# Kernel tuning notes

Hardware: AMD Instinct MI355X
Metric: run time of the kernel (lower is better)

Reference implementation:

```python
import jax, jax.numpy as jnp
import numpy as np

N, D_IN, H, OUT, L = 6144, 512, 512, 256, 3
EPS = 1e-5


def setup_inputs() -> dict:
    key = jax.random.key(0)
    ks = jax.random.split(key, 32)
    inp = {}
    inp["X"] = jax.random.normal(ks[0], (N, D_IN), dtype=jnp.float32)
    inp["adj"] = jax.random.randint(ks[1], (N, N), 0, 2).astype(jnp.float32)
    inp["adj_glo"] = jax.random.randint(ks[2], (N, N), 0, 2).astype(jnp.float32)
    s = 1.0 / np.sqrt(H)
    # projection + its BN
    inp["Wp"] = jax.random.normal(ks[3], (H, D_IN), dtype=jnp.float32) / np.sqrt(D_IN)
    inp["bp"] = jnp.zeros((H,), jnp.float32)
    inp["gp"] = jnp.ones((H,), jnp.float32)
    inp["betap"] = jnp.zeros((H,), jnp.float32)
    # per-layer params; layers 0,1 output H, layer 2 outputs OUT
    outs = [H, H, OUT]
    for i in range(L):
        o = outs[i]
        k = jax.random.split(ks[4 + i], 6)
        inp[f"Wq{i}"] = jax.random.normal(k[0], (H, H), jnp.float32) * s
        inp[f"Wk{i}"] = jax.random.normal(k[1], (H, H), jnp.float32) * s
        inp[f"Wv{i}"] = jax.random.normal(k[2], (H, H), jnp.float32) * s
        inp[f"Wo{i}"] = jax.random.normal(k[3], (o, H), jnp.float32) * s
        inp[f"bo{i}"] = jnp.zeros((o,), jnp.float32)
        inp[f"g{i}"] = jnp.ones((o,), jnp.float32)
        inp[f"beta{i}"] = jnp.zeros((o,), jnp.float32)
    return inp


def _normalize_adj(a):
    # symmetric GCN normalization D^{-1/2} A D^{-1/2}
    d = a.sum(axis=1)
    dis = jnp.where(d > 0, jax.lax.rsqrt(jnp.maximum(d, 1e-12)), 0.0)
    return a * dis[:, None] * dis[None, :]


def _bn(x, g, b):
    # BatchNorm1d, training mode: batch stats, biased variance
    m = x.mean(axis=0)
    v = x.var(axis=0)
    return g * (x - m) * jax.lax.rsqrt(v + EPS) + b


def _attn(h, adj, Wq, Wk, Wv, Wo, bo):
    Q = h @ Wq.T
    K = h @ Wk.T
    V = h @ Wv.T
    scores = (Q @ K.T) / np.sqrt(H)            # [N, N]
    scores = jnp.where(adj == 0, -jnp.inf, scores)
    attn = jax.nn.softmax(scores, axis=-1)
    return (attn @ V) @ Wo.T + bo


def reference(X, adj, adj_glo, Wp, bp, gp, betap,
              Wq0, Wk0, Wv0, Wo0, bo0, g0, beta0,
              Wq1, Wk1, Wv1, Wo1, bo1, g1, beta1,
              Wq2, Wk2, Wv2, Wo2, bo2, g2, beta2):
    # embedding: normalized global adjacency aggregation + projection + BN
    h = _normalize_adj(adj_glo) @ X
    h = h @ Wp.T + bp
    h = _bn(h, gp, betap)
    embed_features = h
    layers = [
        (Wq0, Wk0, Wv0, Wo0, bo0, g0, beta0),
        (Wq1, Wk1, Wv1, Wo1, bo1, g1, beta1),
        (Wq2, Wk2, Wv2, Wo2, bo2, g2, beta2),
    ]
    for i, (Wq, Wk, Wv, Wo, bo, g, b) in enumerate(layers):
        h_s = h
        h = _attn(h, adj, Wq, Wk, Wv, Wo, bo)
        h = jax.nn.relu(_bn(h, g, b))
        if i != L - 1:
            h = h + h_s
    return h, embed_features
```

## Files before the change

### kernel.cpp

```cpp
#include <hip/hip_runtime.h>
#include <cstdint>

#define NROW 6144
#define HDIM 512
#define DOUT 256
#define NEG_INF (-__builtin_inff())

typedef _Float16 half8 __attribute__((ext_vector_type(8)));
typedef _Float16 half4v __attribute__((ext_vector_type(4)));
typedef float f32x4 __attribute__((ext_vector_type(4)));

#define BARRIER() asm volatile("s_barrier" ::: "memory")
#define LGKM0()   asm volatile("s_waitcnt lgkmcnt(0)" ::: "memory")
#define VMCNT4()  asm volatile("s_waitcnt vmcnt(4)" ::: "memory")
#define VMCNT0()  asm volatile("s_waitcnt vmcnt(0)" ::: "memory")

__device__ __forceinline__ void gld_lds16(void* lds, const void* g) {
  __builtin_amdgcn_global_load_lds(
      (const __attribute__((address_space(1))) void*)g,
      (__attribute__((address_space(3))) void*)lds, 16, 0, 0);
}

__global__ __launch_bounds__(512, 2)
void gemm256(const _Float16* __restrict__ A, int lda,
             const _Float16* __restrict__ B, int ldb,
             _Float16* __restrict__ C, int ldc, int Kc, long MN)
{
  __shared__ _Float16 As[2][256][64];
  __shared__ _Float16 Bs[2][256][64];
  const int tid = threadIdx.x;
  const int wave = tid >> 6, lane = tid & 63;
  const int wr = wave >> 2, wc = wave & 3;

  const int gx = gridDim.x, gy = gridDim.y;
  const int nwg = gx * gy * gridDim.z;
  int lin = (blockIdx.z * gy + blockIdx.y) * gx + blockIdx.x;
  int swz = (nwg % 8 == 0) ? ((lin % 8) * (nwg >> 3) + (lin >> 3)) : lin;
  const int bx = swz % gx, by = (swz / gx) % gy, bz = swz / (gx * gy);
  const int row0 = bx * 256, col0 = by * 256;
  const _Float16* Ab = A + (size_t)row0 * lda + (size_t)bz * Kc;
  const _Float16* Bb = B + (size_t)col0 * ldb + (size_t)bz * Kc;
  const int nt = Kc >> 6;

  const int srow = lane >> 3;
  const int sgr  = (lane & 7) ^ srow;

  auto stageA = [&](int buf, int h, int t) {
    const _Float16* src = Ab + (size_t)(h * 128 + wave * 8 + srow) * lda + t * 64 + sgr * 8;
    gld_lds16(&As[buf][h * 128 + wave * 8][0], src);
    gld_lds16(&As[buf][h * 128 + 64 + wave * 8][0], src + (size_t)64 * lda);
  };
  auto stageB = [&](int buf, int h, int t) {
    const _Float16* src = Bb + (size_t)(h * 128 + wave * 8 + srow) * ldb + t * 64 + sgr * 8;
    gld_lds16(&Bs[buf][h * 128 + wave * 8][0], src);
    gld_lds16(&Bs[buf][h * 128 + 64 + wave * 8][0], src + (size_t)64 * ldb);
  };

  const int fr = lane & 15, sq = lane >> 4, fx = fr & 7;
  half8 af[4][2], bLo[2][2], bHi[2][2];
  f32x4 acc[8][4];
  const f32x4 vzero = {0.f, 0.f, 0.f, 0.f};
  #pragma unroll
  for (int f = 0; f < 8; ++f)
    #pragma unroll
    for (int j = 0; j < 4; ++j)
      acc[f][j] = vzero;

  auto dsA = [&](int buf, int mh) {
    #pragma unroll
    for (int i = 0; i < 4; ++i)
      #pragma unroll
      for (int ks = 0; ks < 2; ++ks)
        af[i][ks] = *(const half8*)&As[buf][wr * 128 + mh * 64 + i * 16 + fr]
                                          [((ks * 4 + sq) ^ fx) * 8];
  };
  auto dsBlo = [&](int buf) {
    #pragma unroll
    for (int jj = 0; jj < 2; ++jj)
      #pragma unroll
      for (int ks = 0; ks < 2; ++ks)
        bLo[jj][ks] = *(const half8*)&Bs[buf][wc * 64 + jj * 16 + fr]
                                            [((ks * 4 + sq) ^ fx) * 8];
  };
  auto dsBhi = [&](int buf) {
    #pragma unroll
    for (int jj = 0; jj < 2; ++jj)
      #pragma unroll
      for (int ks = 0; ks < 2; ++ks)
        bHi[jj][ks] = *(const half8*)&Bs[buf][wc * 64 + 32 + jj * 16 + fr]
                                            [((ks * 4 + sq) ^ fx) * 8];
  };
  auto mQlo = [&](int fb) {
    __builtin_amdgcn_s_setprio(1);
    #pragma unroll
    for (int i = 0; i < 4; ++i)
      #pragma unroll
      for (int jj = 0; jj < 2; ++jj)
        #pragma unroll
        for (int ks = 0; ks < 2; ++ks)
          acc[fb + i][jj] = __builtin_amdgcn_mfma_f32_16x16x32_f16(
              af[i][ks], bLo[jj][ks], acc[fb + i][jj], 0, 0, 0);
    __builtin_amdgcn_s_setprio(0);
  };
  auto mQhi = [&](int fb) {
    __builtin_amdgcn_s_setprio(1);
    #pragma unroll
    for (int i = 0; i < 4; ++i)
      #pragma unroll
      for (int jj = 0; jj < 2; ++jj)
        #pragma unroll
        for (int ks = 0; ks < 2; ++ks)
          acc[fb + i][2 + jj] = __builtin_amdgcn_mfma_f32_16x16x32_f16(
              af[i][ks], bHi[jj][ks], acc[fb + i][2 + jj], 0, 0, 0);
    __builtin_amdgcn_s_setprio(0);
  };

  stageA(0, 0, 0); stageA(0, 1, 0); stageB(0, 0, 0); stageB(0, 1, 0);
  stageB(1, 0, 1); stageB(1, 1, 1);
  VMCNT4();
  BARRIER();

  for (int T = 0; T < nt; T += 2) {
    const bool pipe = (T + 2 < nt);
    dsA(0, 0); dsBlo(0);
    stageA(1, 0, T + 1);
    BARRIER(); LGKM0(); mQlo(0); BARRIER();
    dsBhi(0);
    stageA(1, 1, T + 1);
    BARRIER(); LGKM0(); mQhi(0); BARRIER();
    dsA(0, 1);
    if (pipe) stageB(0, 0, T + 2);
    BARRIER(); LGKM0(); mQhi(4); BARRIER();
    if (pipe) { stageB(0, 1, T + 2); VMCNT4(); } else { VMCNT0(); }
    BARRIER(); mQlo(4); BARRIER();
    dsA(1, 0); dsBlo(1);
    if (pipe) stageA(0, 0, T + 2);
    BARRIER(); LGKM0(); mQlo(0); BARRIER();
    dsBhi(1);
    if (pipe) stageA(0, 1, T + 2);
    BARRIER(); LGKM0(); mQhi(0); BARRIER();
    dsA(1, 1);
    if (pipe) stageB(1, 0, T + 3);
    BARRIER(); LGKM0(); mQhi(4); BARRIER();
    if (pipe) { stageB(1, 1, T + 3); VMCNT4(); } else { VMCNT0(); }
    BARRIER(); mQlo(4); BARRIER();
  }

  _Float16* dst = C + (size_t)bz * MN;
  #pragma unroll
  for (int f = 0; f < 8; ++f)
    #pragma unroll
    for (int j = 0; j < 4; ++j)
      #pragma unroll
      for (int r = 0; r < 4; ++r) {
        int row = row0 + wr * 128 + f * 16 + sq * 4 + r;
        int col = col0 + wc * 64 + j * 16 + fr;
        dst[(size_t)row * ldc + col] = (_Float16)acc[f][j][r];
      }
}

__global__ __launch_bounds__(256)
void gemm_f16(const _Float16* __restrict__ A, int lda,
              const _Float16* __restrict__ B, int ldb,
              float* __restrict__ Cf, _Float16* __restrict__ Ch, int ldc,
              int Kc, _Float16* __restrict__ Pk, long MN)
{
  __shared__ _Float16 As[128][32];
  __shared__ _Float16 Bs[128][32];
  const int tid = threadIdx.x;
  const int wave = tid >> 6, lane = tid & 63;
  const int wr = wave >> 1, wc = wave & 1;
  const int row0 = blockIdx.x * 128, col0 = blockIdx.y * 128;
  const int kbase = blockIdx.z * Kc;

  const int sr = lane >> 2;
  const int sk = ((lane & 3) ^ ((lane >> 3) & 3)) * 8;

  f32x4 acc[4][4];
  const f32x4 vzero = {0.f, 0.f, 0.f, 0.f};
  #pragma unroll
  for (int i = 0; i < 4; ++i)
    #pragma unroll
    for (int j = 0; j < 4; ++j)
      acc[i][j] = vzero;

  const int fr = lane & 15;
  const int fk = (((lane >> 4) ^ ((fr >> 1) & 3))) * 8;

  for (int k0 = kbase; k0 < kbase + Kc; k0 += 32) {
    #pragma unroll
    for (int c = 0; c < 2; ++c) {
      int rbase = c * 64 + wave * 16;
      gld_lds16(&As[rbase][0], A + (size_t)(row0 + rbase + sr) * lda + k0 + sk);
      gld_lds16(&Bs[rbase][0], B + (size_t)(col0 + rbase + sr) * ldb + k0 + sk);
    }
    __syncthreads();
    half8 af[4], bf[4];
    #pragma unroll
    for (int i = 0; i < 4; ++i)
      af[i] = *(const half8*)&As[wr * 64 + i * 16 + fr][fk];
    #pragma unroll
    for (int j = 0; j < 4; ++j)
      bf[j] = *(const half8*)&Bs[wc * 64 + j * 16 + fr][fk];
    #pragma unroll
    for (int i = 0; i < 4; ++i)
      #pragma unroll
      for (int j = 0; j < 4; ++j)
        acc[i][j] = __builtin_amdgcn_mfma_f32_16x16x32_f16(af[i], bf[j], acc[i][j], 0, 0, 0);
    __syncthreads();
  }

  const int lr = (lane >> 4) * 4;
  const int lc = lane & 15;
  if (Pk) {
    _Float16* dst = Pk + (size_t)blockIdx.z * MN;
    #pragma unroll
    for (int i = 0; i < 4; ++i)
      #pragma unroll
      for (int j = 0; j < 4; ++j)
        #pragma unroll
        for (int r = 0; r < 4; ++r) {
          int row = row0 + wr * 64 + i * 16 + lr + r;
          int col = col0 + wc * 64 + j * 16 + lc;
          dst[(size_t)row * ldc + col] = (_Float16)acc[i][j][r];
        }
    return;
  }
  #pragma unroll
  for (int i = 0; i < 4; ++i)
    #pragma unroll
    for (int j = 0; j < 4; ++j)
      #pragma unroll
      for (int r = 0; r < 4; ++r) {
        int row = row0 + wr * 64 + i * 16 + lr + r;
        int col = col0 + wc * 64 + j * 16 + lc;
        float v = acc[i][j][r];
        if (Cf) Cf[(size_t)row * ldc + col] = v;
        if (Ch) Ch[(size_t)row * ldc + col] = (_Float16)v;
      }
}

__global__ __launch_bounds__(256)
void pv_exp(const _Float16* __restrict__ S, const _Float16* __restrict__ VT,
            const uint32_t* __restrict__ bits, const float* __restrict__ mrow,
            _Float16* __restrict__ Pk, int Kc, long MN)
{
  __shared__ _Float16 As[128][32];
  __shared__ _Float16 Bs[128][32];
  const int tid = threadIdx.x;
  const int wave = tid >> 6, lane = tid & 63;
  const int wr = wave >> 1, wc = wave & 1;
  const int row0 = blockIdx.x * 128, col0 = blockIdx.y * 128;
  const int kbase = blockIdx.z * Kc;

  const int sr = lane >> 2;
  const int lsl = (lane & 3) ^ ((lane >> 3) & 3);
  const int psl = lane & 3;

  int arow[2]; float mv[2]; const uint32_t* brow[2]; size_t sbase[2];
  #pragma unroll
  for (int c = 0; c < 2; ++c) {
    arow[c] = row0 + c * 64 + wave * 16 + sr;
    mv[c] = mrow[arow[c]];
    brow[c] = bits + (size_t)arow[c] * 192;
    sbase[c] = (size_t)arow[c] * NROW + kbase + lsl * 8;
  }

  f32x4 acc[4][4];
  const f32x4 vzero = {0.f, 0.f, 0.f, 0.f};
  #pragma unroll
  for (int i = 0; i < 4; ++i)
    #pragma unroll
    for (int j = 0; j < 4; ++j)
      acc[i][j] = vzero;

  const int fr = lane & 15;
  const int fk = (((lane >> 4) ^ ((fr >> 1) & 3))) * 8;

  for (int k0 = 0; k0 < Kc; k0 += 32) {
    #pragma unroll
    for (int c = 0; c < 2; ++c) {
      int rbase = c * 64 + wave * 16;
      gld_lds16(&Bs[rbase][0], VT + (size_t)(col0 + rbase + sr) * NROW + kbase + k0 + lsl * 8);
    }
    #pragma unroll
    for (int c = 0; c < 2; ++c) {
      int kv = kbase + k0 + lsl * 8;
      half8 sv = *(const half8*)&S[sbase[c] + k0];
      uint32_t w = (brow[c][kv >> 5] >> (kv & 31)) & 0xffu;
      half8 pvv;
      #pragma unroll
      for (int e = 0; e < 8; ++e)
        pvv[e] = (_Float16)(((w >> e) & 1u) ? __expf((float)sv[e] - mv[c]) : 0.f);
      *(half8*)&As[c * 64 + wave * 16 + sr][psl * 8] = pvv;
    }
    __syncthreads();
    half8 af[4], bf[4];
    #pragma unroll
    for (int i = 0; i < 4; ++i)
      af[i] = *(const half8*)&As[wr * 64 + i * 16 + fr][fk];
    #pragma unroll
    for (int j = 0; j < 4; ++j)
      bf[j] = *(const half8*)&Bs[wc * 64 + j * 16 + fr][fk];
    #pragma unroll
    for (int i = 0; i < 4; ++i)
      #pragma unroll
      for (int j = 0; j < 4; ++j)
        acc[i][j] = __builtin_amdgcn_mfma_f32_16x16x32_f16(af[i], bf[j], acc[i][j], 0, 0, 0);
    __syncthreads();
  }

  const int lr = (lane >> 4) * 4;
  const int lc = lane & 15;
  _Float16* dst = Pk + (size_t)blockIdx.z * MN;
  #pragma unroll
  for (int i = 0; i < 4; ++i)
    #pragma unroll
    for (int j = 0; j < 4; ++j)
      #pragma unroll
      for (int r = 0; r < 4; ++r) {
        int row = row0 + wr * 64 + i * 16 + lr + r;
        int col = col0 + wc * 64 + j * 16 + lc;
        dst[(size_t)row * 512 + col] = (_Float16)acc[i][j][r];
      }
}

__global__ __launch_bounds__(256)
void reduce_splitk(const _Float16* __restrict__ Pk, long MN, int S, int cshift,
                   const float* __restrict__ rowscale,
                   float* __restrict__ Yf, _Float16* __restrict__ Yh)
{
  long n4 = MN >> 2;
  for (long i = (long)blockIdx.x * 256 + threadIdx.x; i < n4; i += (long)gridDim.x * 256) {
    float s0 = 0, s1 = 0, s2 = 0, s3 = 0;
    for (int z = 0; z < S; ++z) {
      half4v p = ((const half4v*)(Pk + (size_t)z * MN))[i];
      s0 += (float)p[0]; s1 += (float)p[1]; s2 += (float)p[2]; s3 += (float)p[3];
    }
    if (rowscale) {
      float sc = rowscale[(i * 4) >> cshift];
      s0 *= sc; s1 *= sc; s2 *= sc; s3 *= sc;
    }
    if (Yf) {
      float4 o; o.x = s0; o.y = s1; o.z = s2; o.w = s3;
      ((float4*)Yf)[i] = o;
    }
    if (Yh) {
      half4v o;
      o[0] = (_Float16)s0; o[1] = (_Float16)s1; o[2] = (_Float16)s2; o[3] = (_Float16)s3;
      ((half4v*)Yh)[i] = o;
    }
  }
}

__global__ __launch_bounds__(256)
void degree_convert(const float* __restrict__ A, _Float16* __restrict__ Ah,
                    float* __restrict__ dis)
{
  const int row = blockIdx.x;
  const float* a = A + (size_t)row * NROW;
  _Float16* o = Ah + (size_t)row * NROW;
  float s = 0.f;
  #pragma unroll
  for (int it = 0; it < 6; ++it) {
    int j = it * 1024 + threadIdx.x * 4;
    float4 v = *(const float4*)&a[j];
    s += v.x + v.y + v.z + v.w;
    half4v h;
    h[0] = (_Float16)v.x; h[1] = (_Float16)v.y; h[2] = (_Float16)v.z; h[3] = (_Float16)v.w;
    *(half4v*)&o[j] = h;
  }
  #pragma unroll
  for (int off = 32; off; off >>= 1) s += __shfl_xor(s, off);
  __shared__ float red[4];
  if ((threadIdx.x & 63) == 0) red[threadIdx.x >> 6] = s;
  __syncthreads();
  if (threadIdx.x == 0) {
    float d = red[0] + red[1] + red[2] + red[3];
    dis[row] = (d > 0.f) ? rsqrtf(fmaxf(d, 1e-12f)) : 0.f;
  }
}

__global__ __launch_bounds__(192)
void build_mask(const float* __restrict__ adj, uint32_t* __restrict__ bits)
{
  const int row = blockIdx.x;
  const int w = threadIdx.x;
  const float* a = adj + (size_t)row * NROW + w * 32;
  uint32_t m = 0;
  #pragma unroll
  for (int q = 0; q < 8; ++q) {
    float4 x = *(const float4*)&a[q * 4];
    m |= (x.x != 0.f ? 1u : 0u) << (q * 4 + 0);
    m |= (x.y != 0.f ? 1u : 0u) << (q * 4 + 1);
    m |= (x.z != 0.f ? 1u : 0u) << (q * 4 + 2);
    m |= (x.w != 0.f ? 1u : 0u) << (q * 4 + 3);
  }
  bits[(size_t)row * 192 + w] = m;
}

struct WConv {
  const float* src[13];
  _Float16* dst[13];
  int n4[13];
  float scale[13];
};
__global__ __launch_bounds__(256)
void convert_weights(WConv w)
{
  const int seg = blockIdx.x >> 4;
  const int bi = blockIdx.x & 15;
  const float* x = w.src[seg];
  _Float16* y = w.dst[seg];
  const float sc = w.scale[seg];
  const int n4 = w.n4[seg];
  for (int i = bi * 256 + threadIdx.x; i < n4; i += 16 * 256) {
    float4 v = ((const float4*)x)[i];
    half4v o;
    o[0] = (_Float16)(v.x * sc); o[1] = (_Float16)(v.y * sc);
    o[2] = (_Float16)(v.z * sc); o[3] = (_Float16)(v.w * sc);
    ((half4v*)y)[i] = o;
  }
}

__global__ __launch_bounds__(256)
void transpose_scale_f16(const float* __restrict__ src, const float* __restrict__ rowscale,
                         _Float16* __restrict__ dst, int R, int C)
{
  __shared__ _Float16 tile[64][72];
  const int c0 = blockIdx.x * 64, r0 = blockIdx.y * 64;
  const int tx4 = (threadIdx.x & 15) * 4, ty = threadIdx.x >> 4;
  #pragma unroll
  for (int p = 0; p < 4; ++p) {
    int r = p * 16 + ty;
    float4 v = *(const float4*)&src[(size_t)(r0 + r) * C + c0 + tx4];
    float sc = rowscale ? rowscale[r0 + r] : 1.0f;
    tile[tx4 + 0][r] = (_Float16)(v.x * sc);
    tile[tx4 + 1][r] = (_Float16)(v.y * sc);
    tile[tx4 + 2][r] = (_Float16)(v.z * sc);
    tile[tx4 + 3][r] = (_Float16)(v.w * sc);
  }
  __syncthreads();
  #pragma unroll
  for (int p = 0; p < 4; ++p) {
    int c = p * 16 + ty;
    half4v o;
    o[0] = tile[c][tx4 + 0];
    o[1] = tile[c][tx4 + 1];
    o[2] = tile[c][tx4 + 2];
    o[3] = tile[c][tx4 + 3];
    *(half4v*)&dst[(size_t)(c0 + c) * R + r0 + tx4] = o;
  }
}

__global__ __launch_bounds__(256)
void transpose_f16(const _Float16* __restrict__ src, int ld,
                   _Float16* __restrict__ dst, int R, int C)
{
  __shared__ _Float16 tile[64][72];
  const int c0 = blockIdx.x * 64, r0 = blockIdx.y * 64;
  const int tx4 = (threadIdx.x & 15) * 4, ty = threadIdx.x >> 4;
  #pragma unroll
  for (int p = 0; p < 4; ++p) {
    int r = p * 16 + ty;
    half4v v = *(const half4v*)&src[(size_t)(r0 + r) * ld + c0 + tx4];
    tile[tx4 + 0][r] = v[0];
    tile[tx4 + 1][r] = v[1];
    tile[tx4 + 2][r] = v[2];
    tile[tx4 + 3][r] = v[3];
  }
  __syncthreads();
  #pragma unroll
  for (int p = 0; p < 4; ++p) {
    int c = p * 16 + ty;
    half4v o;
    o[0] = tile[c][tx4 + 0];
    o[1] = tile[c][tx4 + 1];
    o[2] = tile[c][tx4 + 2];
    o[3] = tile[c][tx4 + 3];
    *(half4v*)&dst[(size_t)(c0 + c) * R + r0 + tx4] = o;
  }
}

__global__ __launch_bounds__(256)
void softmax_stats(const _Float16* __restrict__ Sf, const uint32_t* __restrict__ bits,
                   float* __restrict__ mrow, float* __restrict__ linv)
{
  const int row = blockIdx.x;
  const _Float16* s = Sf + (size_t)row * NROW;
  const uint32_t* b = bits + (size_t)row * 192;
  const int tid = threadIdx.x;
  float v[24];
  float m = NEG_INF;
  #pragma unroll
  for (int it = 0; it < 3; ++it) {
    int j = it * 2048 + tid * 8;
    half8 sv = *(const half8*)&s[j];
    uint32_t w = (b[j >> 5] >> (j & 31)) & 0xffu;
    #pragma unroll
    for (int e = 0; e < 8; ++e) {
      float x = ((w >> e) & 1u) ? (float)sv[e] : NEG_INF;
      v[it * 8 + e] = x;
      m = fmaxf(m, x);
    }
  }
  #pragma unroll
  for (int off = 32; off; off >>= 1) m = fmaxf(m, __shfl_xor(m, off));
  __shared__ float red[4];
  const int lane = tid & 63, wave = tid >> 6;
  if (lane == 0) red[wave] = m;
  __syncthreads();
  m = fmaxf(fmaxf(red[0], red[1]), fmaxf(red[2], red[3]));
  __syncthreads();
  float l = 0.f;
  #pragma unroll
  for (int k = 0; k < 24; ++k)
    l += (v[k] == NEG_INF) ? 0.f : __expf(v[k] - m);
  #pragma unroll
  for (int off = 32; off; off >>= 1) l += __shfl_xor(l, off);
  if (lane == 0) red[wave] = l;
  __syncthreads();
  if (tid == 0) {
    l = red[0] + red[1] + red[2] + red[3];
    mrow[row] = m;
    linv[row] = (l > 0.f) ? (1.f / l) : 0.f;
  }
}

__global__ __launch_bounds__(256)
void bn_partial(const _Float16* __restrict__ X, int C,
                float* __restrict__ psum, float* __restrict__ psq)
{
  const int b = blockIdx.x;
  const int t = threadIdx.x;
  const int tpc = C >> 3;
  const int ng = 256 / tpc;
  const int g = t / tpc, c8 = (t % tpc) * 8;
  const int rpg = 64 / ng;
  const _Float16* x = X + (size_t)b * 64 * C;
  float s[8], q[8];
  #pragma unroll
  for (int e = 0; e < 8; ++e) { s[e] = 0.f; q[e] = 0.f; }
  for (int r = g * rpg; r < (g + 1) * rpg; ++r) {
    half8 v = *(const half8*)&x[(size_t)r * C + c8];
    #pragma unroll
    for (int e = 0; e < 8; ++e) {
      float f = (float)v[e];
      s[e] += f; q[e] += f * f;
    }
  }
  __shared__ float ls[256][8], lq[256][8];
  #pragma unroll
  for (int e = 0; e < 8; ++e) { ls[t][e] = s[e]; lq[t][e] = q[e]; }
  __syncthreads();
  for (int u = t; u < C; u += 256) {
    float ss = 0, qq = 0;
    for (int gg = 0; gg < ng; ++gg) {
      ss += ls[gg * tpc + (u >> 3)][u & 7];
      qq += lq[gg * tpc + (u >> 3)][u & 7];
    }
    psum[b * C + u] = ss; psq[b * C + u] = qq;
  }
}

__global__ void bn_finalize(const float* __restrict__ psum, const float* __restrict__ psq,
                            int C, const float* __restrict__ g, const float* __restrict__ beta,
                            float* __restrict__ scale, float* __restrict__ shift)
{
  int c = threadIdx.x + blockIdx.x * blockDim.x;
  if (c >= C) return;
  float s = 0, q = 0;
  for (int b = 0; b < 96; ++b) { s += psum[b * C + c]; q += psq[b * C + c]; }
  const float invN = 1.0f / 6144.0f;
  float mean = s * invN;
  float var = q * invN - mean * mean;
  float rstd = rsqrtf(fmaxf(var, 0.f) + 1e-5f);
  float sc = g[c] * rstd;
  scale[c] = sc;
  shift[c] = beta[c] - mean * sc;
}

__global__ __launch_bounds__(256)
void bn_apply(const _Float16* __restrict__ X, const float* __restrict__ scale,
              const float* __restrict__ shift, const _Float16* __restrict__ residual,
              float* __restrict__ Yf, _Float16* __restrict__ Yh,
              int Cmask, long total, int do_relu)
{
  for (long i = (long)blockIdx.x * 256 + threadIdx.x; i < total; i += (long)gridDim.x * 256) {
    int c = (int)(i & Cmask);
    float v = (float)X[i] * scale[c] + shift[c];
    if (do_relu) v = fmaxf(v, 0.f);
    if (residual) v += (float)residual[i];
    if (Yf) Yf[i] = v;
    if (Yh) Yh[i] = (_Float16)v;
  }
}

extern "C" void kernel_launch(void* const* d_in, const int* in_sizes, int n_in,
                              void* d_out, int out_size, void* d_ws, size_t ws_size,
                              hipStream_t stream)
{
  (void)in_sizes; (void)n_in; (void)out_size; (void)ws_size;
  const float* X     = (const float*)d_in[0];
  const float* adj   = (const float*)d_in[1];
  const float* adjg  = (const float*)d_in[2];
  const float* Wp    = (const float*)d_in[3];
  const float* gp    = (const float*)d_in[5];
  const float* betap = (const float*)d_in[6];

  float* out_h     = (float*)d_out;
  float* out_embed = out_h + (size_t)NROW * DOUT;

  char* base = (char*)d_ws;
  size_t off = 0;
  auto alloc = [&](size_t bytes) -> void* {
    void* p = base + off;
    off += (bytes + 255) & ~(size_t)255;
    return p;
  };

  const long MN512 = (long)NROW * 512;

  _Float16* Ag  = (_Float16*)alloc((size_t)NROW * NROW * 2);
  _Float16* Sf  = Ag;
  uint32_t* bits = (uint32_t*)alloc((size_t)NROW * 192 * 4);
  _Float16* Pk  = (_Float16*)alloc((size_t)8 * MN512 * 2);
  _Float16* XsT = (_Float16*)alloc((size_t)HDIM * NROW * 2);
  _Float16* Yh16 = (_Float16*)alloc((size_t)NROW * HDIM * 2);
  _Float16* Wph = (_Float16*)alloc((size_t)HDIM * HDIM * 2);
  _Float16* QKVW[3];
  for (int i = 0; i < 3; ++i) QKVW[i] = (_Float16*)alloc((size_t)1536 * HDIM * 2);
  _Float16* Woh[3];
  Woh[0] = (_Float16*)alloc((size_t)512 * 512 * 2);
  Woh[1] = (_Float16*)alloc((size_t)512 * 512 * 2);
  Woh[2] = (_Float16*)alloc((size_t)256 * 512 * 2);
  _Float16* QKVh = (_Float16*)alloc((size_t)NROW * 1536 * 2);
  _Float16* VTh  = (_Float16*)alloc((size_t)HDIM * NROW * 2);
  _Float16* AVh  = (_Float16*)alloc((size_t)NROW * HDIM * 2);
  _Float16* xh   = (_Float16*)alloc((size_t)NROW * HDIM * 2);
  _Float16* hb16A = (_Float16*)alloc((size_t)NROW * HDIM * 2);
  _Float16* hb16B = (_Float16*)alloc((size_t)NROW * HDIM * 2);
  float* dis  = (float*)alloc((size_t)NROW * 4);
  float* mrow = (float*)alloc((size_t)NROW * 4);
  float* linv = (float*)alloc((size_t)NROW * 4);
  float* psum = (float*)alloc((size_t)96 * 512 * 4);
  float* psq  = (float*)alloc((size_t)96 * 512 * 4);
  float* bnsc = (float*)alloc(512 * 4);
  float* bnsh = (float*)alloc(512 * 4);

  const float qk_scale = 0.21022410381342863f;

  degree_convert<<<NROW, 256, 0, stream>>>(adjg, Ag, dis);
  build_mask<<<NROW, 192, 0, stream>>>(adj, bits);
  transpose_scale_f16<<<dim3(8, 96), 256, 0, stream>>>(X, dis, XsT, NROW, HDIM);

  {
    WConv w;
    int seg = 0;
    w.src[seg] = Wp; w.dst[seg] = Wph; w.n4[seg] = 512 * 512 / 4; w.scale[seg] = 1.f; ++seg;
    for (int i = 0; i < 3; ++i) {
      int o = (i < 2) ? 512 : 256;
      w.src[seg] = (const float*)d_in[7 + i * 7 + 0]; w.dst[seg] = QKVW[i];
      w.n4[seg] = 512 * 512 / 4; w.scale[seg] = qk_scale; ++seg;
      w.src[seg] = (const float*)d_in[7 + i * 7 + 1]; w.dst[seg] = QKVW[i] + 512 * 512;
      w.n4[seg] = 512 * 512 / 4; w.scale[seg] = qk_scale; ++seg;
      w.src[seg] = (const float*)d_in[7 + i * 7 + 2]; w.dst[seg] = QKVW[i] + 2 * 512 * 512;
      w.n4[seg] = 512 * 512 / 4; w.scale[seg] = 1.f; ++seg;
      w.src[seg] = (const float*)d_in[7 + i * 7 + 3]; w.dst[seg] = Woh[i];
      w.n4[seg] = o * 512 / 4; w.scale[seg] = 1.f; ++seg;
    }
    convert_weights<<<13 * 16, 256, 0, stream>>>(w);
  }

  gemm256<<<dim3(24, 2, 8), 512, 0, stream>>>(Ag, NROW, XsT, NROW, Pk, 512, 768, MN512);
  reduce_splitk<<<1536, 256, 0, stream>>>(Pk, MN512, 8, 9, dis, nullptr, Yh16);
  gemm_f16<<<dim3(48, 4), 256, 0, stream>>>(Yh16, HDIM, Wph, HDIM, nullptr, xh, HDIM,
                                            512, nullptr, 0);
  bn_partial<<<96, 256, 0, stream>>>(xh, 512, psum, psq);
  bn_finalize<<<2, 256, 0, stream>>>(psum, psq, 512, gp, betap, bnsc, bnsh);
  bn_apply<<<2048, 256, 0, stream>>>(xh, bnsc, bnsh, nullptr, out_embed, hb16A,
                                     511, MN512, 0);

  _Float16* hbuf[2] = {hb16A, hb16B};
  int cur = 0;
  for (int i = 0; i < 3; ++i) {
    int o = (i < 2) ? 512 : 256;
    const float* gl = (const float*)d_in[7 + i * 7 + 5];
    const float* bl = (const float*)d_in[7 + i * 7 + 6];
    _Float16* hin = hbuf[cur];

    gemm_f16<<<dim3(48, 12), 256, 0, stream>>>(hin, HDIM, QKVW[i], HDIM, nullptr, QKVh, 1536,
                                               512, nullptr, 0);
    transpose_f16<<<dim3(8, 96), 256, 0, stream>>>(QKVh + 1024, 1536, VTh, NROW, HDIM);
    gemm256<<<dim3(24, 24), 512, 0, stream>>>(QKVh, 1536, QKVh + 512, 1536, Sf, NROW, 512, 0);
    softmax_stats<<<NROW, 256, 0, stream>>>(Sf, bits, mrow, linv);
    pv_exp<<<dim3(48, 4, 8), 256, 0, stream>>>(Sf, VTh, bits, mrow, Pk, 768, MN512);
    reduce_splitk<<<1536, 256, 0, stream>>>(Pk, MN512, 8, 9, linv, nullptr, AVh);
    long MNo = (long)NROW * o;
    gemm_f16<<<dim3(48, o / 128, 4), 256, 0, stream>>>(AVh, HDIM, Woh[i], HDIM,
                                                       nullptr, nullptr, o, 128, Pk, MNo);
    reduce_splitk<<<1536, 256, 0, stream>>>(Pk, MNo, 4, (o == 512) ? 9 : 8, nullptr,
                                            nullptr, xh);
    bn_partial<<<96, 256, 0, stream>>>(xh, o, psum, psq);
    bn_finalize<<<2, 256, 0, stream>>>(psum, psq, o, gl, bl, bnsc, bnsh);
    if (i < 2) {
      bn_apply<<<2048, 256, 0, stream>>>(xh, bnsc, bnsh, hin, nullptr, hbuf[cur ^ 1],
                                         o - 1, (long)NROW * o, 1);
      cur ^= 1;
    } else {
      bn_apply<<<2048, 256, 0, stream>>>(xh, bnsc, bnsh, nullptr, out_h, nullptr,
                                         o - 1, (long)NROW * o, 1);
    }
  }
}
```

Measured before the change: 901.2 us.

## Materialize masked exp scores in softmax pass and use gemm256 for PV

The softmax stats kernel now writes the masked, max-shifted exponentials back into the fp16 score buffer instead of only recording the row max. The PV product then runs on the generic 256-tile gemm256 kernel with split-K, replacing the custom pv_exp kernel that recomputed exp and mask bits inside its load loop. This moves exp work out of the GEMM inner loop and lets PV use the faster tuned GEMM, at the cost of an extra full write of the N×N fp16 score matrix.

```diff
diff --git a/kernel.cpp b/kernel.cpp
--- a/kernel.cpp
+++ b/kernel.cpp
@@ -241,91 +241,6 @@
 }
 
 __global__ __launch_bounds__(256)
-void pv_exp(const _Float16* __restrict__ S, const _Float16* __restrict__ VT,
-            const uint32_t* __restrict__ bits, const float* __restrict__ mrow,
-            _Float16* __restrict__ Pk, int Kc, long MN)
-{
-  __shared__ _Float16 As[128][32];
-  __shared__ _Float16 Bs[128][32];
-  const int tid = threadIdx.x;
-  const int wave = tid >> 6, lane = tid & 63;
-  const int wr = wave >> 1, wc = wave & 1;
-  const int row0 = blockIdx.x * 128, col0 = blockIdx.y * 128;
-  const int kbase = blockIdx.z * Kc;
-
-  const int sr = lane >> 2;
-  const int lsl = (lane & 3) ^ ((lane >> 3) & 3);
-  const int psl = lane & 3;
-
-  int arow[2]; float mv[2]; const uint32_t* brow[2]; size_t sbase[2];
-  #pragma unroll
-  for (int c = 0; c < 2; ++c) {
-    arow[c] = row0 + c * 64 + wave * 16 + sr;
-    mv[c] = mrow[arow[c]];
-    brow[c] = bits + (size_t)arow[c] * 192;
-    sbase[c] = (size_t)arow[c] * NROW + kbase + lsl * 8;
-  }
-
-  f32x4 acc[4][4];
-  const f32x4 vzero = {0.f, 0.f, 0.f, 0.f};
-  #pragma unroll
-  for (int i = 0; i < 4; ++i)
-    #pragma unroll
-    for (int j = 0; j < 4; ++j)
-      acc[i][j] = vzero;
-
-  const int fr = lane & 15;
-  const int fk = (((lane >> 4) ^ ((fr >> 1) & 3))) * 8;
-
-  for (int k0 = 0; k0 < Kc; k0 += 32) {
-    #pragma unroll
-    for (int c = 0; c < 2; ++c) {
-      int rbase = c * 64 + wave * 16;
-      gld_lds16(&Bs[rbase][0], VT + (size_t)(col0 + rbase + sr) * NROW + kbase + k0 + lsl * 8);
-    }
-    #pragma unroll
-    for (int c = 0; c < 2; ++c) {
-      int kv = kbase + k0 + lsl * 8;
-      half8 sv = *(const half8*)&S[sbase[c] + k0];
-      uint32_t w = (brow[c][kv >> 5] >> (kv & 31)) & 0xffu;
-      half8 pvv;
-      #pragma unroll
-      for (int e = 0; e < 8; ++e)
-        pvv[e] = (_Float16)(((w >> e) & 1u) ? __expf((float)sv[e] - mv[c]) : 0.f);
-      *(half8*)&As[c * 64 + wave * 16 + sr][psl * 8] = pvv;
-    }
-    __syncthreads();
-    half8 af[4], bf[4];
-    #pragma unroll
-    for (int i = 0; i < 4; ++i)
-      af[i] = *(const half8*)&As[wr * 64 + i * 16 + fr][fk];
-    #pragma unroll
-    for (int j = 0; j < 4; ++j)
-      bf[j] = *(const half8*)&Bs[wc * 64 + j * 16 + fr][fk];
-    #pragma unroll
-    for (int i = 0; i < 4; ++i)
-      #pragma unroll
-      for (int j = 0; j < 4; ++j)
-        acc[i][j] = __builtin_amdgcn_mfma_f32_16x16x32_f16(af[i], bf[j], acc[i][j], 0, 0, 0);
-    __syncthreads();
-  }
-
-  const int lr = (lane >> 4) * 4;
-  const int lc = lane & 15;
-  _Float16* dst = Pk + (size_t)blockIdx.z * MN;
-  #pragma unroll
-  for (int i = 0; i < 4; ++i)
-    #pragma unroll
-    for (int j = 0; j < 4; ++j)
-      #pragma unroll
-      for (int r = 0; r < 4; ++r) {
-        int row = row0 + wr * 64 + i * 16 + lr + r;
-        int col = col0 + wc * 64 + j * 16 + lc;
-        dst[(size_t)row * 512 + col] = (_Float16)acc[i][j][r];
-      }
-}
-
-__global__ __launch_bounds__(256)
 void reduce_splitk(const _Float16* __restrict__ Pk, long MN, int S, int cshift,
                    const float* __restrict__ rowscale,
                    float* __restrict__ Yf, _Float16* __restrict__ Yh)
@@ -483,11 +398,11 @@
 }
 
 __global__ __launch_bounds__(256)
-void softmax_stats(const _Float16* __restrict__ Sf, const uint32_t* __restrict__ bits,
-                   float* __restrict__ mrow, float* __restrict__ linv)
+void softmax_mask16(_Float16* __restrict__ Sf, const uint32_t* __restrict__ bits,
+                    float* __restrict__ linv)
 {
   const int row = blockIdx.x;
-  const _Float16* s = Sf + (size_t)row * NROW;
+  _Float16* s = Sf + (size_t)row * NROW;
   const uint32_t* b = bits + (size_t)row * 192;
   const int tid = threadIdx.x;
   float v[24];
@@ -514,16 +429,23 @@
   __syncthreads();
   float l = 0.f;
   #pragma unroll
-  for (int k = 0; k < 24; ++k)
-    l += (v[k] == NEG_INF) ? 0.f : __expf(v[k] - m);
+  for (int k = 0; k < 24; ++k) {
+    float e = (v[k] == NEG_INF) ? 0.f : __expf(v[k] - m);
+    v[k] = e; l += e;
+  }
   #pragma unroll
   for (int off = 32; off; off >>= 1) l += __shfl_xor(l, off);
   if (lane == 0) red[wave] = l;
   __syncthreads();
-  if (tid == 0) {
-    l = red[0] + red[1] + red[2] + red[3];
-    mrow[row] = m;
-    linv[row] = (l > 0.f) ? (1.f / l) : 0.f;
+  l = red[0] + red[1] + red[2] + red[3];
+  if (tid == 0) linv[row] = (l > 0.f) ? (1.f / l) : 0.f;
+  #pragma unroll
+  for (int it = 0; it < 3; ++it) {
+    int j = it * 2048 + tid * 8;
+    half8 o;
+    #pragma unroll
+    for (int e = 0; e < 8; ++e) o[e] = (_Float16)v[it * 8 + e];
+    *(half8*)&s[j] = o;
   }
 }
 
@@ -641,7 +563,6 @@
   _Float16* hb16A = (_Float16*)alloc((size_t)NROW * HDIM * 2);
   _Float16* hb16B = (_Float16*)alloc((size_t)NROW * HDIM * 2);
   float* dis  = (float*)alloc((size_t)NROW * 4);
-  float* mrow = (float*)alloc((size_t)NROW * 4);
   float* linv = (float*)alloc((size_t)NROW * 4);
   float* psum = (float*)alloc((size_t)96 * 512 * 4);
   float* psq  = (float*)alloc((size_t)96 * 512 * 4);
@@ -693,8 +614,8 @@
                                                512, nullptr, 0);
     transpose_f16<<<dim3(8, 96), 256, 0, stream>>>(QKVh + 1024, 1536, VTh, NROW, HDIM);
     gemm256<<<dim3(24, 24), 512, 0, stream>>>(QKVh, 1536, QKVh + 512, 1536, Sf, NROW, 512, 0);
-    softmax_stats<<<NROW, 256, 0, stream>>>(Sf, bits, mrow, linv);
-    pv_exp<<<dim3(48, 4, 8), 256, 0, stream>>>(Sf, VTh, bits, mrow, Pk, 768, MN512);
+    softmax_mask16<<<NROW, 256, 0, stream>>>(Sf, bits, linv);
+    gemm256<<<dim3(24, 2, 8), 512, 0, stream>>>(Sf, NROW, VTh, NROW, Pk, 512, 768, MN512);
     reduce_splitk<<<1536, 256, 0, stream>>>(Pk, MN512, 8, 9, linv, nullptr, AVh);
     long MNo = (long)NROW * o;
     gemm_f16<<<dim3(48, o / 128, 4), 256, 0, stream>>>(AVh, HDIM, Woh[i], HDIM,
```

After: 834.7 us. 1.08x faster.
